# Kernel tuning notes

Measured on AMD Instinct MI355X. Metric: run time of the kernel, lower is better.

The kernel has to match this reference:

```python
import jax, jax.numpy as jnp
import numpy as np

B, S, D = 2048, 200, 192  # batch, seq_len, total_dim
H1, H2 = 64, 32
IN = 4 * D


def prelu(x, a):
    return jnp.where(x >= 0, x, a * x)


def setup_inputs() -> dict:
    key = jax.random.key(0)
    ks = jax.random.split(key, 10)
    scale = lambda fan_in: 1.0 / np.sqrt(fan_in)
    return {
        "query": jax.random.normal(ks[0], (B, D), jnp.float32),
        "keys": jax.random.normal(ks[1], (B, S, D), jnp.float32),
        "keys_mask": jax.random.randint(ks[2], (B, S), 0, 2, jnp.int32),
        "W1": jax.random.uniform(ks[3], (IN, H1), jnp.float32, -scale(IN), scale(IN)),
        "b1": jnp.zeros((H1,), jnp.float32),
        "a1": jnp.asarray(0.25, jnp.float32),  # PReLU default slope
        "W2": jax.random.uniform(ks[4], (H1, H2), jnp.float32, -scale(H1), scale(H1)),
        "b2": jnp.zeros((H2,), jnp.float32),
        "a2": jnp.asarray(0.25, jnp.float32),
        "W3": jax.random.uniform(ks[5], (H2, 1), jnp.float32, -scale(H2), scale(H2)),
        "b3": jnp.zeros((1,), jnp.float32),
    }


def reference(query, keys, keys_mask, W1, b1, a1, W2, b2, a2, W3, b3):
    q = query[:, None, :]  # [B,1,D] broadcasts against keys [B,S,D]
    qe = jnp.broadcast_to(q, keys.shape)
    x = jnp.concatenate([keys, qe, keys * qe, keys - qe], axis=-1)  # [B,S,4D]
    h = prelu(jnp.einsum("bsi,ih->bsh", x, W1) + b1, a1)
    h = prelu(jnp.einsum("bsh,hk->bsk", h, W2) + b2, a2)
    scores = (jnp.einsum("bsk,ko->bso", h, W3) + b3)[..., 0]  # [B,S]
    scores = jnp.where(keys_mask.astype(bool), scores, -jnp.inf)
    w = jax.nn.softmax(scores, axis=-1)
    w = jnp.where(jnp.isnan(w), jnp.zeros_like(w), w)
    weighted_sum = jnp.einsum("bs,bsd->bd", w, keys)
    return weighted_sum, w
```

## Files before the change

kernel.cpp:

```cpp
#include <hip/hip_runtime.h>


#define B_N 2048
#define S_N 200
#define D_N 192

typedef __bf16 bf16x8 __attribute__((ext_vector_type(8)));
typedef __bf16 bf16x4 __attribute__((ext_vector_type(4)));
typedef float  f32x4  __attribute__((ext_vector_type(4)));

struct __align__(16) Smem {
  unsigned char kbuf[32*400];
  unsigned char h1buf[32*144];
  unsigned char w2t[32*144];
  float h2buf[32*36];
  float qbuf[192];
  float cbuf[64];
  float cpart[4][64];
  float scores[224];
  int   maskbuf[224];
  float p_lds[32];
  float w3buf[32];
  float b2buf[32];
  float consts[4];
  float sm_m, sm_l, sm_factor;
};

__global__ __launch_bounds__(256, 4) void rich_attn_kernel(
    const float* __restrict__ query, const float* __restrict__ keys,
    const int*   __restrict__ keys_mask, const float* __restrict__ W1,
    const float* __restrict__ b1, const float* __restrict__ a1,
    const float* __restrict__ W2, const float* __restrict__ b2,
    const float* __restrict__ a2, const float* __restrict__ W3,
    const float* __restrict__ b3, float* __restrict__ out)
{
  __shared__ Smem sm;
  const int tid  = threadIdx.x;
  const int b    = blockIdx.x;
  const int wave = tid >> 6;
  const int quad = (tid >> 4) & 3;
  const int n16  = tid & 15;

  if (tid < 192) sm.qbuf[tid] = query[b*D_N + tid];
  if (tid < 224) sm.maskbuf[tid] = (tid < 200) ? keys_mask[b*S_N + tid] : 0;
  if (tid < 32)  sm.w3buf[tid] = W3[tid];
  if (tid >= 32 && tid < 64) sm.b2buf[tid-32] = b2[tid-32];
  if (tid == 64) { sm.consts[0] = a1[0]; sm.consts[1] = a2[0]; sm.consts[2] = b3[0]; }
  if (tid == 65) { sm.sm_m = -1e30f; sm.sm_l = 0.f; sm.sm_factor = 1.f; }
  for (int i = tid; i < 64*32; i += 256) {
    int hh = i >> 5, kk = i & 31;
    *((__bf16*)&sm.w2t[kk*144 + hh*2]) = (__bf16)W2[i];
  }
  __syncthreads();

  {
    int hh = tid & 63, pp = tid >> 6;
    float acc = 0.f;
    int d0 = pp*48;
    #pragma unroll 4
    for (int d = d0; d < d0+48; ++d)
      acc += sm.qbuf[d] * (W1[(192+d)*64 + hh] - W1[(576+d)*64 + hh]);
    sm.cpart[pp][hh] = acc;
  }
  bf16x8 fb1[6];
  {
    int h = (wave << 4) | n16;
    #pragma unroll
    for (int t = 0; t < 6; ++t) {
      #pragma unroll
      for (int j = 0; j < 8; ++j) {
        int d = t*32 + quad*8 + j;
        float v = W1[d*64 + h] + W1[(576+d)*64 + h] + sm.qbuf[d]*W1[(384+d)*64 + h];
        fb1[t][j] = (__bf16)v;
      }
    }
  }
  const int mt2 = wave & 1, nt2 = wave >> 1;
  bf16x8 fw2[2];
  #pragma unroll
  for (int t = 0; t < 2; ++t)
    fw2[t] = *(const bf16x8*)&sm.w2t[(nt2*16 + n16)*144 + (t*32 + quad*8)*2];
  __syncthreads();
  if (tid < 64)
    sm.cbuf[tid] = b1[tid] + sm.cpart[0][tid] + sm.cpart[1][tid]
                 + sm.cpart[2][tid] + sm.cpart[3][tid];

  const float* kb = keys + (size_t)b * (S_N * D_N);
  f32x4 o = {0.f, 0.f, 0.f, 0.f};

  for (int tile = 0; tile < 7; ++tile) {
    const int s0 = tile * 32;
    #pragma unroll
    for (int i = 0; i < 6; ++i) {
      int f = tid + i*256;
      int row = f / 48, c4 = f % 48;
      int sg = s0 + row;
      float4 v = make_float4(0.f, 0.f, 0.f, 0.f);
      if (sg < 200) v = ((const float4*)kb)[sg*48 + c4];
      bf16x4 bv; bv[0]=(__bf16)v.x; bv[1]=(__bf16)v.y; bv[2]=(__bf16)v.z; bv[3]=(__bf16)v.w;
      *(bf16x4*)&sm.kbuf[row*400 + c4*8] = bv;
    }
    __syncthreads();

    f32x4 acc1[2];
    acc1[0] = (f32x4){0.f,0.f,0.f,0.f};
    acc1[1] = (f32x4){0.f,0.f,0.f,0.f};
    #pragma unroll
    for (int t = 0; t < 6; ++t) {
      #pragma unroll
      for (int mt = 0; mt < 2; ++mt) {
        bf16x8 fa = *(const bf16x8*)&sm.kbuf[(mt*16 + n16)*400 + (t*32 + quad*8)*2];
        acc1[mt] = __builtin_amdgcn_mfma_f32_16x16x32_bf16(fa, fb1[t], acc1[mt], 0, 0, 0);
      }
    }
    {
      float a1v = sm.consts[0];
      int h = (wave << 4) | n16;
      float cb = sm.cbuf[h];
      #pragma unroll
      for (int mt = 0; mt < 2; ++mt) {
        #pragma unroll
        for (int r = 0; r < 4; ++r) {
          int m = mt*16 + quad*4 + r;
          float v = acc1[mt][r] + cb;
          v = (v >= 0.f) ? v : a1v * v;
          *((__bf16*)&sm.h1buf[m*144 + h*2]) = (__bf16)v;
        }
      }
    }
    __syncthreads();

    {
      f32x4 acc2 = {0.f,0.f,0.f,0.f};
      #pragma unroll
      for (int t = 0; t < 2; ++t) {
        bf16x8 fa = *(const bf16x8*)&sm.h1buf[(mt2*16 + n16)*144 + (t*32 + quad*8)*2];
        acc2 = __builtin_amdgcn_mfma_f32_16x16x32_bf16(fa, fw2[t], acc2, 0, 0, 0);
      }
      float a2v = sm.consts[1];
      int k2 = nt2*16 + n16;
      float bb = sm.b2buf[k2];
      #pragma unroll
      for (int r = 0; r < 4; ++r) {
        int m = mt2*16 + quad*4 + r;
        float v = acc2[r] + bb;
        v = (v >= 0.f) ? v : a2v * v;
        sm.h2buf[m*36 + k2] = v;
      }
    }
    __syncthreads();

    if (tid < 32) {
      int s = tid;
      float sc = sm.consts[2];
      #pragma unroll
      for (int k = 0; k < 32; k += 4) {
        f32x4 hv = *(const f32x4*)&sm.h2buf[s*36 + k];
        sc += hv[0]*sm.w3buf[k] + hv[1]*sm.w3buf[k+1] + hv[2]*sm.w3buf[k+2] + hv[3]*sm.w3buf[k+3];
      }
      int sg = s0 + s;
      bool valid = (sg < 200) && (sm.maskbuf[sg] != 0);
      sc = valid ? sc : -1e30f;
      sm.scores[sg] = sc;
      float mt_ = sc;
      #pragma unroll
      for (int off = 1; off < 32; off <<= 1) mt_ = fmaxf(mt_, __shfl_xor(mt_, off, 64));
      float m_old = sm.sm_m;
      float m_new = fmaxf(m_old, mt_);
      float fac = __expf(m_old - m_new);
      float p = valid ? __expf(sc - m_new) : 0.f;
      sm.p_lds[s] = p;
      float ps = p;
      #pragma unroll
      for (int off = 1; off < 32; off <<= 1) ps += __shfl_xor(ps, off, 64);
      if (s == 0) { sm.sm_m = m_new; sm.sm_l = sm.sm_l*fac + ps; sm.sm_factor = fac; }
    }
    if (tid < 48) {
      float fac = sm.sm_factor;
      o[0] *= fac; o[1] *= fac; o[2] *= fac; o[3] *= fac;
      #pragma unroll 8
      for (int s2 = 0; s2 < 32; ++s2) {
        float p = sm.p_lds[s2];
        bf16x4 kv = *(const bf16x4*)&sm.kbuf[s2*400 + tid*8];
        o[0] += p * (float)kv[0];
        o[1] += p * (float)kv[1];
        o[2] += p * (float)kv[2];
        o[3] += p * (float)kv[3];
      }
    }
    __syncthreads();
  }

  float l = sm.sm_l;
  float m = sm.sm_m;
  float invl = (l > 0.f) ? 1.f / l : 0.f;
  if (tid < 200) {
    float wv = (l > 0.f) ? __expf(sm.scores[tid] - m) * invl : 0.f;
    out[(size_t)B_N * D_N + (size_t)b * S_N + tid] = wv;
  }
  if (tid < 48) {
    f32x4 res = { o[0]*invl, o[1]*invl, o[2]*invl, o[3]*invl };
    *(f32x4*)&out[(size_t)b * D_N + tid*4] = res;
  }
}

extern "C" void kernel_launch(void* const* d_in, const int* in_sizes, int n_in,
                              void* d_out, int out_size, void* d_ws, size_t ws_size,
                              hipStream_t stream) {
  const float* query     = (const float*)d_in[0];
  const float* keys      = (const float*)d_in[1];
  const int*   keys_mask = (const int*)  d_in[2];
  const float* W1        = (const float*)d_in[3];
  const float* b1        = (const float*)d_in[4];
  const float* a1        = (const float*)d_in[5];
  const float* W2        = (const float*)d_in[6];
  const float* b2        = (const float*)d_in[7];
  const float* a2        = (const float*)d_in[8];
  const float* W3        = (const float*)d_in[9];
  const float* b3        = (const float*)d_in[10];
  float* out = (float*)d_out;
  rich_attn_kernel<<<dim3(B_N), dim3(256), 0, stream>>>(
      query, keys, keys_mask, W1, b1, a1, W2, b2, a2, W3, b3, out);
}
```

Measured before the change: 559.8 us.

## Use 64-row tiles with per-wave fused layer2/score/softmax and final merge

Tiles grow from 32 to 64 sequence rows, so there are 4 iterations instead of 7. Each wave now owns 16 rows through layer 2, computes the W3 dot product in registers via shuffles, and keeps its own online-softmax state. All four waves accumulate the weighted key sum, and the partial results are merged across waves at the end. This removes the h2 LDS round trip, the serial single-wave softmax stage, and two barriers per tile. In exchange it uses more LDS and registers, and occupancy is lowered to 3 blocks per CU.

```diff
diff --git a/kernel.cpp b/kernel.cpp
--- a/kernel.cpp
+++ b/kernel.cpp
@@ -10,23 +10,22 @@
 typedef float  f32x4  __attribute__((ext_vector_type(4)));
 
 struct __align__(16) Smem {
-  unsigned char kbuf[32*400];
-  unsigned char h1buf[32*144];
+  unsigned char kbuf[64*400];
+  unsigned char h1buf[64*144];
   unsigned char w2t[32*144];
-  float h2buf[32*36];
   float qbuf[192];
   float cbuf[64];
   float cpart[4][64];
-  float scores[224];
-  int   maskbuf[224];
-  float p_lds[32];
+  float scores[256];
+  int   maskbuf[256];
+  float opart[4][192];
+  float wm[4], wl[4];
   float w3buf[32];
   float b2buf[32];
   float consts[4];
-  float sm_m, sm_l, sm_factor;
 };
 
-__global__ __launch_bounds__(256, 4) void rich_attn_kernel(
+__global__ __launch_bounds__(256, 3) void rich_attn_kernel(
     const float* __restrict__ query, const float* __restrict__ keys,
     const int*   __restrict__ keys_mask, const float* __restrict__ W1,
     const float* __restrict__ b1, const float* __restrict__ a1,
@@ -38,15 +37,15 @@
   const int tid  = threadIdx.x;
   const int b    = blockIdx.x;
   const int wave = tid >> 6;
+  const int lane = tid & 63;
   const int quad = (tid >> 4) & 3;
   const int n16  = tid & 15;
 
   if (tid < 192) sm.qbuf[tid] = query[b*D_N + tid];
-  if (tid < 224) sm.maskbuf[tid] = (tid < 200) ? keys_mask[b*S_N + tid] : 0;
+  sm.maskbuf[tid] = (tid < 200) ? keys_mask[b*S_N + tid] : 0;
   if (tid < 32)  sm.w3buf[tid] = W3[tid];
-  if (tid >= 32 && tid < 64) sm.b2buf[tid-32] = b2[tid-32];
+  else if (tid < 64) sm.b2buf[tid-32] = b2[tid-32];
   if (tid == 64) { sm.consts[0] = a1[0]; sm.consts[1] = a2[0]; sm.consts[2] = b3[0]; }
-  if (tid == 65) { sm.sm_m = -1e30f; sm.sm_l = 0.f; sm.sm_factor = 1.f; }
   for (int i = tid; i < 64*32; i += 256) {
     int hh = i >> 5, kk = i & 31;
     *((__bf16*)&sm.w2t[kk*144 + hh*2]) = (__bf16)W2[i];
@@ -75,23 +74,28 @@
       }
     }
   }
-  const int mt2 = wave & 1, nt2 = wave >> 1;
-  bf16x8 fw2[2];
+  bf16x8 fw2[2][2];
   #pragma unroll
-  for (int t = 0; t < 2; ++t)
-    fw2[t] = *(const bf16x8*)&sm.w2t[(nt2*16 + n16)*144 + (t*32 + quad*8)*2];
+  for (int nt2 = 0; nt2 < 2; ++nt2)
+    #pragma unroll
+    for (int t = 0; t < 2; ++t)
+      fw2[nt2][t] = *(const bf16x8*)&sm.w2t[(nt2*16 + n16)*144 + (t*32 + quad*8)*2];
+  const float w3v0 = sm.w3buf[n16],      w3v1 = sm.w3buf[16 + n16];
+  const float bbv0 = sm.b2buf[n16],      bbv1 = sm.b2buf[16 + n16];
+  const float a1v = sm.consts[0], a2v = sm.consts[1], b3v = sm.consts[2];
   __syncthreads();
   if (tid < 64)
     sm.cbuf[tid] = b1[tid] + sm.cpart[0][tid] + sm.cpart[1][tid]
                  + sm.cpart[2][tid] + sm.cpart[3][tid];
 
   const float* kb = keys + (size_t)b * (S_N * D_N);
+  float m_run = -1e30f, l_run = 0.f;
   f32x4 o = {0.f, 0.f, 0.f, 0.f};
 
-  for (int tile = 0; tile < 7; ++tile) {
-    const int s0 = tile * 32;
-    #pragma unroll
-    for (int i = 0; i < 6; ++i) {
+  for (int tile = 0; tile < 4; ++tile) {
+    const int s0 = tile * 64;
+    #pragma unroll
+    for (int i = 0; i < 12; ++i) {
       int f = tid + i*256;
       int row = f / 48, c4 = f % 48;
       int sg = s0 + row;
@@ -102,23 +106,21 @@
     }
     __syncthreads();
 
-    f32x4 acc1[2];
-    acc1[0] = (f32x4){0.f,0.f,0.f,0.f};
-    acc1[1] = (f32x4){0.f,0.f,0.f,0.f};
-    #pragma unroll
-    for (int t = 0; t < 6; ++t) {
-      #pragma unroll
-      for (int mt = 0; mt < 2; ++mt) {
+    f32x4 acc1[4];
+    #pragma unroll
+    for (int mt = 0; mt < 4; ++mt) acc1[mt] = (f32x4){0.f,0.f,0.f,0.f};
+    #pragma unroll
+    for (int mt = 0; mt < 4; ++mt)
+      #pragma unroll
+      for (int t = 0; t < 6; ++t) {
         bf16x8 fa = *(const bf16x8*)&sm.kbuf[(mt*16 + n16)*400 + (t*32 + quad*8)*2];
         acc1[mt] = __builtin_amdgcn_mfma_f32_16x16x32_bf16(fa, fb1[t], acc1[mt], 0, 0, 0);
       }
-    }
     {
-      float a1v = sm.consts[0];
       int h = (wave << 4) | n16;
       float cb = sm.cbuf[h];
       #pragma unroll
-      for (int mt = 0; mt < 2; ++mt) {
+      for (int mt = 0; mt < 4; ++mt)
         #pragma unroll
         for (int r = 0; r < 4; ++r) {
           int m = mt*16 + quad*4 + r;
@@ -126,81 +128,97 @@
           v = (v >= 0.f) ? v : a1v * v;
           *((__bf16*)&sm.h1buf[m*144 + h*2]) = (__bf16)v;
         }
+    }
+    __syncthreads();
+
+    bf16x8 fa2[2];
+    #pragma unroll
+    for (int t = 0; t < 2; ++t)
+      fa2[t] = *(const bf16x8*)&sm.h1buf[(wave*16 + n16)*144 + (t*32 + quad*8)*2];
+    f32x4 acc2[2];
+    acc2[0] = (f32x4){0.f,0.f,0.f,0.f};
+    acc2[1] = (f32x4){0.f,0.f,0.f,0.f};
+    #pragma unroll
+    for (int nt2 = 0; nt2 < 2; ++nt2)
+      #pragma unroll
+      for (int t = 0; t < 2; ++t)
+        acc2[nt2] = __builtin_amdgcn_mfma_f32_16x16x32_bf16(fa2[t], fw2[nt2][t], acc2[nt2], 0, 0, 0);
+
+    float sc[4];
+    #pragma unroll
+    for (int r = 0; r < 4; ++r) {
+      float v0 = acc2[0][r] + bbv0; v0 = (v0 >= 0.f) ? v0 : a2v * v0;
+      float v1 = acc2[1][r] + bbv1; v1 = (v1 >= 0.f) ? v1 : a2v * v1;
+      sc[r] = v0 * w3v0 + v1 * w3v1;
+    }
+    #pragma unroll
+    for (int off = 1; off < 16; off <<= 1)
+      #pragma unroll
+      for (int r = 0; r < 4; ++r) sc[r] += __shfl_xor(sc[r], off);
+
+    float p[4];
+    float mloc = -1e30f;
+    #pragma unroll
+    for (int r = 0; r < 4; ++r) {
+      int sg = s0 + wave*16 + quad*4 + r;
+      sc[r] += b3v;
+      bool valid = (sg < 200) && (sm.maskbuf[sg] != 0);
+      sc[r] = valid ? sc[r] : -1e30f;
+      mloc = fmaxf(mloc, sc[r]);
+    }
+    if (n16 == 0) {
+      #pragma unroll
+      for (int r = 0; r < 4; ++r) sm.scores[s0 + wave*16 + quad*4 + r] = sc[r];
+    }
+    mloc = fmaxf(mloc, __shfl_xor(mloc, 16));
+    mloc = fmaxf(mloc, __shfl_xor(mloc, 32));
+    float m_new = fmaxf(m_run, mloc);
+    float fac = __expf(m_run - m_new);
+    float psum = 0.f;
+    #pragma unroll
+    for (int r = 0; r < 4; ++r) {
+      p[r] = (sc[r] > -1e29f) ? __expf(sc[r] - m_new) : 0.f;
+      psum += p[r];
+    }
+    psum += __shfl_xor(psum, 16);
+    psum += __shfl_xor(psum, 32);
+    l_run = l_run * fac + psum;
+    m_run = m_new;
+
+    float pv[16];
+    #pragma unroll
+    for (int s2 = 0; s2 < 16; ++s2)
+      pv[s2] = __shfl(p[s2 & 3], (s2 >> 2) * 16);
+    o[0] *= fac; o[1] *= fac; o[2] *= fac; o[3] *= fac;
+    if (lane < 48) {
+      #pragma unroll
+      for (int s2 = 0; s2 < 16; ++s2) {
+        bf16x4 kv = *(const bf16x4*)&sm.kbuf[(wave*16 + s2)*400 + lane*8];
+        o[0] += pv[s2] * (float)kv[0];
+        o[1] += pv[s2] * (float)kv[1];
+        o[2] += pv[s2] * (float)kv[2];
+        o[3] += pv[s2] * (float)kv[3];
       }
     }
     __syncthreads();
-
-    {
-      f32x4 acc2 = {0.f,0.f,0.f,0.f};
-      #pragma unroll
-      for (int t = 0; t < 2; ++t) {
-        bf16x8 fa = *(const bf16x8*)&sm.h1buf[(mt2*16 + n16)*144 + (t*32 + quad*8)*2];
-        acc2 = __builtin_amdgcn_mfma_f32_16x16x32_bf16(fa, fw2[t], acc2, 0, 0, 0);
-      }
-      float a2v = sm.consts[1];
-      int k2 = nt2*16 + n16;
-      float bb = sm.b2buf[k2];
-      #pragma unroll
-      for (int r = 0; r < 4; ++r) {
-        int m = mt2*16 + quad*4 + r;
-        float v = acc2[r] + bb;
-        v = (v >= 0.f) ? v : a2v * v;
-        sm.h2buf[m*36 + k2] = v;
-      }
-    }
-    __syncthreads();
-
-    if (tid < 32) {
-      int s = tid;
-      float sc = sm.consts[2];
-      #pragma unroll
-      for (int k = 0; k < 32; k += 4) {
-        f32x4 hv = *(const f32x4*)&sm.h2buf[s*36 + k];
-        sc += hv[0]*sm.w3buf[k] + hv[1]*sm.w3buf[k+1] + hv[2]*sm.w3buf[k+2] + hv[3]*sm.w3buf[k+3];
-      }
-      int sg = s0 + s;
-      bool valid = (sg < 200) && (sm.maskbuf[sg] != 0);
-      sc = valid ? sc : -1e30f;
-      sm.scores[sg] = sc;
-      float mt_ = sc;
-      #pragma unroll
-      for (int off = 1; off < 32; off <<= 1) mt_ = fmaxf(mt_, __shfl_xor(mt_, off, 64));
-      float m_old = sm.sm_m;
-      float m_new = fmaxf(m_old, mt_);
-      float fac = __expf(m_old - m_new);
-      float p = valid ? __expf(sc - m_new) : 0.f;
-      sm.p_lds[s] = p;
-      float ps = p;
-      #pragma unroll
-      for (int off = 1; off < 32; off <<= 1) ps += __shfl_xor(ps, off, 64);
-      if (s == 0) { sm.sm_m = m_new; sm.sm_l = sm.sm_l*fac + ps; sm.sm_factor = fac; }
-    }
-    if (tid < 48) {
-      float fac = sm.sm_factor;
-      o[0] *= fac; o[1] *= fac; o[2] *= fac; o[3] *= fac;
-      #pragma unroll 8
-      for (int s2 = 0; s2 < 32; ++s2) {
-        float p = sm.p_lds[s2];
-        bf16x4 kv = *(const bf16x4*)&sm.kbuf[s2*400 + tid*8];
-        o[0] += p * (float)kv[0];
-        o[1] += p * (float)kv[1];
-        o[2] += p * (float)kv[2];
-        o[3] += p * (float)kv[3];
-      }
-    }
-    __syncthreads();
-  }
-
-  float l = sm.sm_l;
-  float m = sm.sm_m;
-  float invl = (l > 0.f) ? 1.f / l : 0.f;
+  }
+
+  if (lane == 0) { sm.wm[wave] = m_run; sm.wl[wave] = l_run; }
+  if (lane < 48) *(f32x4*)&sm.opart[wave][lane*4] = o;
+  __syncthreads();
+  float mg = fmaxf(fmaxf(sm.wm[0], sm.wm[1]), fmaxf(sm.wm[2], sm.wm[3]));
+  float e0 = __expf(sm.wm[0] - mg), e1 = __expf(sm.wm[1] - mg);
+  float e2 = __expf(sm.wm[2] - mg), e3 = __expf(sm.wm[3] - mg);
+  float lg = sm.wl[0]*e0 + sm.wl[1]*e1 + sm.wl[2]*e2 + sm.wl[3]*e3;
+  float invl = (lg > 0.f) ? 1.f / lg : 0.f;
+  if (tid < 192) {
+    float os = sm.opart[0][tid]*e0 + sm.opart[1][tid]*e1
+             + sm.opart[2][tid]*e2 + sm.opart[3][tid]*e3;
+    out[(size_t)b * D_N + tid] = os * invl;
+  }
   if (tid < 200) {
-    float wv = (l > 0.f) ? __expf(sm.scores[tid] - m) * invl : 0.f;
+    float wv = (lg > 0.f) ? __expf(sm.scores[tid] - mg) * invl : 0.f;
     out[(size_t)B_N * D_N + (size_t)b * S_N + tid] = wv;
-  }
-  if (tid < 48) {
-    f32x4 res = { o[0]*invl, o[1]*invl, o[2]*invl, o[3]*invl };
-    *(f32x4*)&out[(size_t)b * D_N + tid*4] = res;
   }
 }
 
```

After: 548.9 us. About the same (-2.0%).
